# Performance work log

Measured on AMD Instinct MI355X. Metric: run time of the kernel, lower is better.

## Reference

```python
import jax, jax.numpy as jnp
import numpy as np

K = 100
TEMPERATURE = 1.0


def setup_inputs() -> dict:
    key = jax.random.key(0)
    k1, k2, k3 = jax.random.split(key, 3)
    student_emb = jax.random.normal(k1, (8, 512, 1500), dtype=jnp.float32)
    teacher_codes = jax.random.randint(k2, (8, 1500), 0, 4096, dtype=jnp.int64)
    codebook = jax.random.normal(k3, (4096, 512), dtype=jnp.float32)
    return {"student_emb": student_emb, "teacher_codes": teacher_codes, "codebook": codebook}


def reference(student_emb, teacher_codes, codebook):
    B, C, T = student_emb.shape
    # flatten tokens: (N, C) with N = B*T
    emb = jnp.transpose(student_emb, (0, 2, 1)).reshape(-1, C)
    codes = teacher_codes.reshape(-1).astype(jnp.int32)

    # Euclidean cdist via the ||a||^2 + ||b||^2 - 2ab expansion (same math as torch.cdist)
    emb_sq = jnp.sum(emb * emb, axis=1, keepdims=True)            # (N,1)
    cb_sq = jnp.sum(codebook * codebook, axis=1)[None, :]         # (1,V)
    d2 = emb_sq + cb_sq - 2.0 * jnp.matmul(emb, codebook.T)       # (N,V)
    distances = jnp.sqrt(jnp.maximum(d2, 0.0))

    # top-k smallest distances
    _, top_k_indices = jax.lax.top_k(-distances, K)               # (N,K)

    # include_correct: replace last candidate with the true code if absent
    correct_in_topk = jnp.any(top_k_indices == codes[:, None], axis=1)
    top_k_indices = top_k_indices.at[:, -1].set(
        jnp.where(correct_in_topk, top_k_indices[:, -1], codes))

    candidate_distances = jnp.take_along_axis(distances, top_k_indices, axis=1)
    logits = -candidate_distances / TEMPERATURE                   # (N,K)

    match = top_k_indices == codes[:, None]
    local_labels = jnp.argmax(match.astype(jnp.int32), axis=1)    # (N,)

    logp = jax.nn.log_softmax(logits, axis=1)
    loss = -jnp.mean(jnp.take_along_axis(logp, local_labels[:, None], axis=1))

    local_predictions = jnp.argmax(logits, axis=-1)
    local_accuracy = jnp.mean((local_predictions == local_labels).astype(jnp.float32))
    global_predictions = jnp.argmin(distances, axis=-1)
    global_accuracy = jnp.mean((global_predictions == codes).astype(jnp.float32))
    correct_in_candidates = jnp.mean(jnp.any(top_k_indices == codes[:, None], axis=1).astype(jnp.float32))

    return loss, local_accuracy, global_accuracy, correct_in_candidates
```

## Files before the change

kernel.cpp:

```cpp
#include <hip/hip_runtime.h>
#include <hip/hip_bf16.h>
#include <cstdint>

#define B_ 8
#define C_ 512
#define T_ 1500
#define N_ (B_*T_)
#define NPAD_ 12032
#define V_ 4096
#define K_ 100

typedef unsigned long long u64;
typedef __attribute__((ext_vector_type(8))) short short8;
typedef __attribute__((ext_vector_type(8))) unsigned short u16x8;
typedef __attribute__((ext_vector_type(4))) float f32x4;

__device__ __forceinline__ unsigned short f2bf(float x){
    __hip_bfloat16 h = __float2bfloat16(x);
    return __builtin_bit_cast(unsigned short, h);
}
__device__ __forceinline__ unsigned short f2h(float x){
    return __builtin_bit_cast(unsigned short, (_Float16)x);
}
__device__ __forceinline__ float h2f(unsigned short h){
    return (float)__builtin_bit_cast(_Float16, h);
}

__device__ __forceinline__ void gll16(const unsigned short* g, unsigned short* l){
    __builtin_amdgcn_global_load_lds(
        (const __attribute__((address_space(1))) void*)g,
        (__attribute__((address_space(3))) void*)l, 16, 0, 0);
}

__global__ __launch_bounds__(256) void cbconv_kernel(const float* __restrict__ CB,
                                                     unsigned short* __restrict__ CBh,
                                                     float* __restrict__ csq){
    int wv = threadIdx.x >> 6, lane = threadIdx.x & 63;
    int r = blockIdx.x * 4 + wv;
    const float4* p4 = (const float4*)(CB + (size_t)r * C_);
    ushort4* o4 = (ushort4*)(CBh + (size_t)r * C_);
    float s = 0.f;
    #pragma unroll
    for (int j = 0; j < 2; ++j){
        float4 v = p4[lane + j*64];
        s += v.x*v.x + v.y*v.y + v.z*v.z + v.w*v.w;
        ushort4 h; h.x = f2bf(v.x); h.y = f2bf(v.y); h.z = f2bf(v.z); h.w = f2bf(v.w);
        o4[lane + j*64] = h;
    }
    #pragma unroll
    for (int o = 32; o; o >>= 1) s += __shfl_down(s, o, 64);
    if (lane == 0) csq[r] = s;
}

__global__ __launch_bounds__(256) void transpose_conv_kernel(const float* __restrict__ S,
                                                             unsigned short* __restrict__ embT,
                                                             float* __restrict__ esq){
    __shared__ float tile[32][33];
    __shared__ float psum[8][33];
    int b  = blockIdx.z;
    int c0 = blockIdx.y * 32;
    int t0 = blockIdx.x * 32;
    int tx = threadIdx.x, ty = threadIdx.y;
    #pragma unroll
    for (int r = 0; r < 4; ++r){
        int c = c0 + ty + r*8;
        int t = t0 + tx;
        tile[ty + r*8][tx] = (t < T_) ? S[((size_t)b*C_ + c)*T_ + t] : 0.f;
    }
    __syncthreads();
    float ps = 0.f;
    #pragma unroll
    for (int r = 0; r < 4; ++r){ float v = tile[ty + r*8][tx]; ps += v * v; }
    psum[ty][tx] = ps;
    #pragma unroll
    for (int r = 0; r < 4; ++r){
        int t = t0 + ty + r*8;
        int c = c0 + tx;
        if (t < T_) embT[((size_t)b*T_ + t)*C_ + c] = f2bf(tile[tx][ty + r*8]);
    }
    __syncthreads();
    if (ty == 0){
        int t = t0 + tx;
        if (t < T_){
            float s2 = 0.f;
            #pragma unroll
            for (int w = 0; w < 8; ++w) s2 += psum[w][tx];
            atomicAdd(&esq[b*T_ + t], s2);
        }
    }
}

__global__ __launch_bounds__(256) void gemm_dot_kernel(
    const unsigned short* __restrict__ A, const unsigned short* __restrict__ Bm,
    unsigned short* __restrict__ doth, int row_lo, int row_hi)
{
    __shared__ unsigned short As[3][128*32];
    __shared__ unsigned short Bs[3][128*32];
    int tid = threadIdx.x, lane = tid & 63, wv = tid >> 6;
    int row0 = row_lo + blockIdx.x * 128;
    int col0 = blockIdx.y * 128;

    int sr = lane >> 2;
    int sk = (lane & 3) * 8;
    int ar0 = row0 + wv*32 + sr;       int ar1 = ar0 + 16;
    int ca0 = (ar0 < N_) ? ar0 : N_-1; int ca1 = (ar1 < N_) ? ar1 : N_-1;
    const unsigned short* Ap0 = A  + (size_t)ca0 * C_ + sk;
    const unsigned short* Ap1 = A  + (size_t)ca1 * C_ + sk;
    const unsigned short* Bp0 = Bm + (size_t)(col0 + wv*32 + sr) * C_ + sk;
    const unsigned short* Bp1 = Bp0 + (size_t)16 * C_;

    int wm = (wv >> 1) * 64, wn = (wv & 1) * 64;
    int fr = lane & 15;
    int fk = (lane >> 4) * 8;

    f32x4 acc[4][4];
    #pragma unroll
    for (int i = 0; i < 4; ++i)
        #pragma unroll
        for (int j = 0; j < 4; ++j) acc[i][j] = (f32x4){0.f, 0.f, 0.f, 0.f};

    auto stage = [&](int s, int kt){
        int k0 = kt * 32;
        gll16(Ap0 + k0, &As[s][(wv*32     ) * 32]);
        gll16(Ap1 + k0, &As[s][(wv*32 + 16) * 32]);
        gll16(Bp0 + k0, &Bs[s][(wv*32     ) * 32]);
        gll16(Bp1 + k0, &Bs[s][(wv*32 + 16) * 32]);
    };
    auto compute = [&](int s){
        short8 af[4], bf[4];
        #pragma unroll
        for (int i = 0; i < 4; ++i) af[i] = *(const short8*)&As[s][(wm + i*16 + fr)*32 + fk];
        #pragma unroll
        for (int j = 0; j < 4; ++j) bf[j] = *(const short8*)&Bs[s][(wn + j*16 + fr)*32 + fk];
        #pragma unroll
        for (int i = 0; i < 4; ++i)
            #pragma unroll
            for (int j = 0; j < 4; ++j)
                acc[i][j] = __builtin_amdgcn_mfma_f32_16x16x32_bf16(bf[j], af[i], acc[i][j], 0, 0, 0);
    };

    stage(0, 0);
    stage(1, 1);

    #pragma unroll
    for (int kt = 0; kt < 14; ++kt){
        asm volatile("s_waitcnt vmcnt(4)" ::: "memory");
        __builtin_amdgcn_s_barrier();
        asm volatile("" ::: "memory");
        stage((kt + 2) % 3, kt + 2);
        compute(kt % 3);
    }
    asm volatile("s_waitcnt vmcnt(4)" ::: "memory");
    __builtin_amdgcn_s_barrier();
    asm volatile("" ::: "memory");
    compute(14 % 3);
    asm volatile("s_waitcnt vmcnt(0)" ::: "memory");
    __builtin_amdgcn_s_barrier();
    asm volatile("" ::: "memory");
    compute(15 % 3);

    int en = lane & 15;
    int ev = (lane >> 4) * 4;
    #pragma unroll
    for (int i = 0; i < 4; ++i){
        int n = row0 + wm + i*16 + en;
        if (n >= row_hi) continue;
        size_t base = (size_t)(n - row_lo) * V_;
        int vb = col0 + wn + ev;
        #pragma unroll
        for (int j = 0; j < 4; ++j){
            ushort4 h;
            h.x = f2h(acc[i][j][0]);
            h.y = f2h(acc[i][j][1]);
            h.z = f2h(acc[i][j][2]);
            h.w = f2h(acc[i][j][3]);
            *(ushort4*)&doth[base + vb + j*16] = h;
        }
    }
}

__global__ __launch_bounds__(256, 2) void select_kernel(const unsigned short* __restrict__ doth,
                                                        const int* __restrict__ codes,
                                                        const float* __restrict__ esq,
                                                        const float* __restrict__ csq,
                                                        float2* __restrict__ pairbuf,
                                                        int row_lo, int nrows){
    int tid = threadIdx.x, lane = tid & 63, wv = tid >> 6;
    int lrow = blockIdx.x * 4 + wv;
    if (lrow >= nrows) return;
    int n = row_lo + lrow;
    const u16x8* r8 = (const u16x8*)(doth + (size_t)lrow * V_);

    __shared__ unsigned hist[4][256] __attribute__((aligned(16)));
    __shared__ unsigned coll[4][64];
    __shared__ unsigned collcnt[4];

    float esq_n = esq[n];
    int code = codes[n];
    float dotc = h2f(doth[(size_t)lrow * V_ + code]);
    unsigned ucode = __float_as_uint(fmaxf(esq_n + csq[code] - 2.f * dotc, 0.f));

    unsigned u[64];
    #pragma unroll
    for (int j = 0; j < 8; ++j){
        u16x8 h = r8[lane + j*64];
        const float4* cp = (const float4*)(csq + 8*lane + 512*j);
        float4 c0 = cp[0], c1 = cp[1];
        float cs[8] = {c0.x, c0.y, c0.z, c0.w, c1.x, c1.y, c1.z, c1.w};
        #pragma unroll
        for (int e = 0; e < 8; ++e){
            float d2 = fmaxf(esq_n + cs[e] - 2.f * h2f(h[e]), 0.f);
            u[8*j+e] = __float_as_uint(d2);
        }
    }

    unsigned umin = u[0], umax = u[0];
    #pragma unroll
    for (int k = 1; k < 64; ++k){
        umin = (u[k] < umin) ? u[k] : umin;
        umax = (u[k] > umax) ? u[k] : umax;
    }
    #pragma unroll
    for (int o = 32; o; o >>= 1){
        unsigned a = (unsigned)__shfl_xor((int)umin, o, 64); if (a < umin) umin = a;
        unsigned b = (unsigned)__shfl_xor((int)umax, o, 64); if (b > umax) umax = b;
    }
    unsigned im = 0xFFFFFFFFu;
    #pragma unroll
    for (int k = 0; k < 64; ++k){
        unsigned idx = 8u*(unsigned)lane + (unsigned)(512*(k >> 3) + (k & 7));
        if (u[k] == umin && idx < im) im = idx;
    }
    #pragma unroll
    for (int o = 32; o; o >>= 1){
        unsigned a = (unsigned)__shfl_xor((int)im, o, 64); if (a < im) im = a;
    }
    int idx0 = (int)im;
    float d0 = sqrtf(__uint_as_float(umin));

    unsigned t;
    if (umin == umax){
        t = umin;
    } else {
        ((uint4*)&hist[wv][0])[lane] = (uint4){0u,0u,0u,0u};
        if (lane == 0) collcnt[wv] = 0u;
        asm volatile("s_waitcnt lgkmcnt(0)" ::: "memory");
        float fmn = __uint_as_float(umin), fmx = __uint_as_float(umax);
        float invw = 256.0f / (fmx - fmn);
        #pragma unroll
        for (int k = 0; k < 64; ++k){
            float fk = __uint_as_float(u[k]);
            int b = (int)((fk - fmn) * invw); b = (b > 255) ? 255 : b;
            atomicAdd(&hist[wv][b], 1u);
        }
        asm volatile("s_waitcnt lgkmcnt(0)" ::: "memory");
        uint4 hq = ((uint4*)&hist[wv][0])[lane];
        unsigned lsum = hq.x + hq.y + hq.z + hq.w;
        unsigned inc = lsum;
        #pragma unroll
        for (int o = 1; o < 64; o <<= 1){
            unsigned y = (unsigned)__shfl_up((int)inc, o, 64);
            if (lane >= o) inc += y;
        }
        unsigned e0 = inc - lsum;
        unsigned e1 = e0 + hq.x, e2 = e1 + hq.y, e3 = e2 + hq.z, e4 = e3 + hq.w;
        int sel = -1;
        if      (e0 <= 99u && 99u < e1) sel = 0;
        else if (e1 <= 99u && 99u < e2) sel = 1;
        else if (e2 <= 99u && 99u < e3) sel = 2;
        else if (e3 <= 99u && 99u < e4) sel = 3;
        u64 bal = __ballot(sel >= 0);
        int src = __ffsll(bal) - 1;
        unsigned myBk = (unsigned)(4*lane + (sel < 0 ? 0 : sel));
        unsigned myBase = (sel == 1) ? e1 : (sel == 2) ? e2 : (sel == 3) ? e3 : e0;
        int Bk   = __shfl((int)myBk,   src, 64);
        int base = __shfl((int)myBase, src, 64);
        int rk = 99 - base;
        #pragma unroll
        for (int k = 0; k < 64; ++k){
            float fk = __uint_as_float(u[k]);
            int b = (int)((fk - fmn) * invw); b = (b > 255) ? 255 : b;
            if (b == Bk){
                unsigned pos = atomicAdd(&collcnt[wv], 1u);
                if (pos < 64u) coll[wv][pos] = u[k];
            }
        }
        asm volatile("s_waitcnt lgkmcnt(0)" ::: "memory");
        unsigned bcnt = collcnt[wv];
        if (bcnt <= 64u){
            unsigned w = (lane < (int)bcnt) ? coll[wv][lane] : 0xFFFFFFFFu;
            unsigned wmn = (lane < (int)bcnt) ? w : 0xFFFFFFFFu;
            unsigned wmx = (lane < (int)bcnt) ? w : 0u;
            #pragma unroll
            for (int o = 32; o; o >>= 1){
                unsigned a = (unsigned)__shfl_xor((int)wmn, o, 64); if (a < wmn) wmn = a;
                unsigned b = (unsigned)__shfl_xor((int)wmx, o, 64); if (b > wmx) wmx = b;
            }
            unsigned P;
            if (wmn == wmx) P = wmn;
            else {
                int hb = 31 - __clz((int)(wmn ^ wmx));
                unsigned mask = (hb == 31) ? 0xFFFFFFFFu : ((1u << (hb+1)) - 1u);
                P = wmn & ~mask;
                for (int b = hb; b >= 0; --b){
                    unsigned cand = P | (1u << b);
                    int c = __popcll(__ballot(w < cand));
                    if (c <= rk) P = cand;
                }
            }
            t = P;
        } else {
            int hb = 31 - __clz((int)(umin ^ umax));
            unsigned mask = (hb == 31) ? 0xFFFFFFFFu : ((1u << (hb+1)) - 1u);
            unsigned P = umin & ~mask;
            for (int b = hb; b >= 0; --b){
                unsigned cand = P | (1u << b);
                int c = 0;
                #pragma unroll
                for (int k = 0; k < 64; ++k) c += (u[k] < cand) ? 1 : 0;
                #pragma unroll
                for (int o = 32; o; o >>= 1) c += __shfl_xor(c, o, 64);
                if (c <= 99) P = cand;
            }
            t = P;
        }
    }
    float tval = sqrtf(__uint_as_float(t));

    float s = 0.f; int cl = 0;
    #pragma unroll
    for (int k = 0; k < 64; ++k){
        if (u[k] < t){ s += __expf(d0 - sqrtf(__uint_as_float(u[k]))); cl++; }
    }
    #pragma unroll
    for (int o = 32; o; o >>= 1){
        s += __shfl_xor(s, o, 64);
        cl += __shfl_xor(cl, o, 64);
    }
    if (lane == 0){
        float S = s + (float)(K_ - cl) * __expf(d0 - tval);
        float dcode = sqrtf(__uint_as_float(ucode));
        if (ucode > t) S += __expf(d0 - dcode) - __expf(d0 - tval);
        float nll = dcode - d0 + __logf(S);
        pairbuf[n] = make_float2(nll, (idx0 == code) ? 1.f : 0.f);
    }
}

__global__ __launch_bounds__(1024) void finalize_kernel(const float2* __restrict__ pair,
                                                        float* __restrict__ out){
    int tid = threadIdx.x;
    float sn = 0.f, sh = 0.f;
    for (int i = tid; i < N_; i += 1024){
        float2 p = pair[i]; sn += p.x; sh += p.y;
    }
    #pragma unroll
    for (int o = 32; o; o >>= 1){ sn += __shfl_down(sn, o, 64); sh += __shfl_down(sh, o, 64); }
    __shared__ float a[16], b[16];
    int wv = tid >> 6, lane = tid & 63;
    if (lane == 0){ a[wv] = sn; b[wv] = sh; }
    __syncthreads();
    if (tid == 0){
        float L = 0.f, H = 0.f;
        #pragma unroll
        for (int i = 0; i < 16; ++i){ L += a[i]; H += b[i]; }
        out[0] = L / (float)N_;
        out[1] = H / (float)N_;
        out[2] = H / (float)N_;
        out[3] = 1.0f;
    }
}

extern "C" void kernel_launch(void* const* d_in, const int* in_sizes, int n_in,
                              void* d_out, int out_size, void* d_ws, size_t ws_size,
                              hipStream_t stream){
    const float* S   = (const float*)d_in[0];
    const int* codes = (const int*)d_in[1];
    const float* CB  = (const float*)d_in[2];
    float* out = (float*)d_out;

    char* w = (char*)d_ws;
    size_t off = 0;
    unsigned short* embT = (unsigned short*)(w + off); off += (size_t)NPAD_ * C_ * 2;
    unsigned short* CBh  = (unsigned short*)(w + off); off += (size_t)V_ * C_ * 2;
    float* csq = (float*)(w + off); off += (size_t)V_ * 4;
    float* esq = (float*)(w + off); off += (size_t)N_ * 4;
    off = (off + 255) & ~(size_t)255;
    float2* pairbuf = (float2*)(w + off); off += (size_t)N_ * 8;
    unsigned short* dotbuf = (unsigned short*)(w + off);

    size_t avail = (ws_size > off) ? ws_size - off : 0;
    long maxrows = (long)(avail / ((size_t)V_ * 2));
    int chunk = (maxrows >= N_) ? N_ : (int)maxrows;
    if (chunk < 4) chunk = 4;

    hipMemsetAsync(esq, 0, (size_t)N_ * 4, stream);
    hipLaunchKernelGGL(cbconv_kernel, dim3(V_/4), dim3(256), 0, stream, CB, CBh, csq);
    hipLaunchKernelGGL(transpose_conv_kernel, dim3((T_+31)/32, C_/32, B_), dim3(32, 8), 0, stream,
                       S, embT, esq);

    for (int row_lo = 0; row_lo < N_; row_lo += chunk){
        int row_hi = row_lo + chunk; if (row_hi > N_) row_hi = N_;
        int rows = row_hi - row_lo;
        hipLaunchKernelGGL(gemm_dot_kernel, dim3((rows + 127)/128, V_/128), dim3(256), 0, stream,
                           embT, CBh, dotbuf, row_lo, row_hi);
        hipLaunchKernelGGL(select_kernel, dim3((rows + 3)/4), dim3(256), 0, stream,
                           dotbuf, codes, esq, csq, pairbuf, row_lo, rows);
    }
    hipLaunchKernelGGL(finalize_kernel, dim3(1), dim3(1024), 0, stream, pairbuf, out);
}
```

Measured before the change: 229.6 us.

## Enlarge GEMM tile to 256x256 with 8 waves, swizzled LDS and 4-stage pipeline

The bf16 distance GEMM moves from 128x128 tiles with 4 waves to 256x256 tiles with 8 waves, each wave computing a 128x64 sub-tile. It uses 128 KB of dynamic LDS with a 4-slot ring and an XOR swizzle on the k offset to avoid bank conflicts. Loads for A and B are interleaved between two half-MFMA phases, with barriers and s_setprio. The aim is better operand reuse and more MFMA issue relative to memory traffic. In exchange, the larger tile gives fewer blocks on a 12000-row problem, so partial tiles and wave quantization may hurt, along with higher register pressure and more barriers.

```diff
diff --git a/kernel.cpp b/kernel.cpp
--- a/kernel.cpp
+++ b/kernel.cpp
@@ -90,83 +90,99 @@
     }
 }
 
-__global__ __launch_bounds__(256) void gemm_dot_kernel(
+__global__ __launch_bounds__(512, 2) void gemm_dot_kernel(
     const unsigned short* __restrict__ A, const unsigned short* __restrict__ Bm,
     unsigned short* __restrict__ doth, int row_lo, int row_hi)
 {
-    __shared__ unsigned short As[3][128*32];
-    __shared__ unsigned short Bs[3][128*32];
+    extern __shared__ unsigned short lds[];
     int tid = threadIdx.x, lane = tid & 63, wv = tid >> 6;
-    int row0 = row_lo + blockIdx.x * 128;
-    int col0 = blockIdx.y * 128;
-
-    int sr = lane >> 2;
-    int sk = (lane & 3) * 8;
-    int ar0 = row0 + wv*32 + sr;       int ar1 = ar0 + 16;
-    int ca0 = (ar0 < N_) ? ar0 : N_-1; int ca1 = (ar1 < N_) ? ar1 : N_-1;
-    const unsigned short* Ap0 = A  + (size_t)ca0 * C_ + sk;
-    const unsigned short* Ap1 = A  + (size_t)ca1 * C_ + sk;
-    const unsigned short* Bp0 = Bm + (size_t)(col0 + wv*32 + sr) * C_ + sk;
-    const unsigned short* Bp1 = Bp0 + (size_t)16 * C_;
-
-    int wm = (wv >> 1) * 64, wn = (wv & 1) * 64;
+    int wm = wv >> 2, wn = wv & 3;
+    int row0 = row_lo + blockIdx.x * 256;
+    int col0 = blockIdx.y * 256;
+
+    int l2 = lane >> 2;
+    int swz = (((lane & 3) ^ (l2 & 3) ^ ((lane >> 4) & 3)) << 3);
+    const unsigned short* ApS[2]; const unsigned short* BpS[2];
+    #pragma unroll
+    for (int r = 0; r < 2; ++r){
+        int ra = row0 + r*128 + wv*16 + l2;
+        int ca = (ra < N_) ? ra : N_-1;
+        ApS[r] = A  + (size_t)ca * C_ + swz;
+        BpS[r] = Bm + (size_t)(col0 + r*128 + wv*16 + l2) * C_ + swz;
+    }
+
     int fr = lane & 15;
-    int fk = (lane >> 4) * 8;
-
-    f32x4 acc[4][4];
-    #pragma unroll
-    for (int i = 0; i < 4; ++i)
+    int q  = lane >> 4;
+    int rsw = ((q ^ (fr & 3) ^ ((fr >> 2) & 3)) << 3);
+    int aBase = (wm*128 + fr)*32 + rsw;
+    int bBase = 32768 + (wn*64 + fr)*32 + rsw;
+
+    f32x4 acc[8][4];
+    #pragma unroll
+    for (int i = 0; i < 8; ++i)
         #pragma unroll
         for (int j = 0; j < 4; ++j) acc[i][j] = (f32x4){0.f, 0.f, 0.f, 0.f};
 
-    auto stage = [&](int s, int kt){
-        int k0 = kt * 32;
-        gll16(Ap0 + k0, &As[s][(wv*32     ) * 32]);
-        gll16(Ap1 + k0, &As[s][(wv*32 + 16) * 32]);
-        gll16(Bp0 + k0, &Bs[s][(wv*32     ) * 32]);
-        gll16(Bp1 + k0, &Bs[s][(wv*32 + 16) * 32]);
+    auto stageA = [&](int kt){
+        int s = kt & 3, k0 = kt * 32;
+        gll16(ApS[0] + k0, &lds[s*8192 +        wv*512]);
+        gll16(ApS[1] + k0, &lds[s*8192 + 4096 + wv*512]);
     };
-    auto compute = [&](int s){
-        short8 af[4], bf[4];
-        #pragma unroll
-        for (int i = 0; i < 4; ++i) af[i] = *(const short8*)&As[s][(wm + i*16 + fr)*32 + fk];
-        #pragma unroll
-        for (int j = 0; j < 4; ++j) bf[j] = *(const short8*)&Bs[s][(wn + j*16 + fr)*32 + fk];
+    auto stageB = [&](int kt){
+        int s = kt & 3, k0 = kt * 32;
+        gll16(BpS[0] + k0, &lds[32768 + s*8192 +        wv*512]);
+        gll16(BpS[1] + k0, &lds[32768 + s*8192 + 4096 + wv*512]);
+    };
+
+    stageA(0); stageB(0);
+    stageA(1); stageB(1);
+    asm volatile("s_waitcnt vmcnt(4)" ::: "memory");
+    __builtin_amdgcn_s_barrier();
+
+    auto tile = [&](int kt, bool doStage, int vm){
+        int s = kt & 3;
+        const unsigned short* Al = &lds[s*8192 + aBase];
+        const unsigned short* Bl = &lds[s*8192 + bBase];
+        short8 a[4], b[4];
+        #pragma unroll
+        for (int j = 0; j < 4; ++j) b[j] = *(const short8*)(Bl + j*512);
+        #pragma unroll
+        for (int i = 0; i < 4; ++i) a[i] = *(const short8*)(Al + i*512);
+        if (doStage) stageA(kt + 2);
+        __builtin_amdgcn_s_barrier();
+        __builtin_amdgcn_s_setprio(1);
         #pragma unroll
         for (int i = 0; i < 4; ++i)
             #pragma unroll
             for (int j = 0; j < 4; ++j)
-                acc[i][j] = __builtin_amdgcn_mfma_f32_16x16x32_bf16(bf[j], af[i], acc[i][j], 0, 0, 0);
+                acc[i][j] = __builtin_amdgcn_mfma_f32_16x16x32_bf16(b[j], a[i], acc[i][j], 0, 0, 0);
+        __builtin_amdgcn_s_setprio(0);
+        __builtin_amdgcn_s_barrier();
+        #pragma unroll
+        for (int i = 0; i < 4; ++i) a[i] = *(const short8*)(Al + (4+i)*512);
+        if (doStage) stageB(kt + 2);
+        if (vm == 4) asm volatile("s_waitcnt vmcnt(4)" ::: "memory");
+        else if (vm == 0) asm volatile("s_waitcnt vmcnt(0)" ::: "memory");
+        __builtin_amdgcn_s_barrier();
+        __builtin_amdgcn_s_setprio(1);
+        #pragma unroll
+        for (int i = 0; i < 4; ++i)
+            #pragma unroll
+            for (int j = 0; j < 4; ++j)
+                acc[4+i][j] = __builtin_amdgcn_mfma_f32_16x16x32_bf16(b[j], a[i], acc[4+i][j], 0, 0, 0);
+        __builtin_amdgcn_s_setprio(0);
+        __builtin_amdgcn_s_barrier();
     };
 
-    stage(0, 0);
-    stage(1, 1);
-
-    #pragma unroll
-    for (int kt = 0; kt < 14; ++kt){
-        asm volatile("s_waitcnt vmcnt(4)" ::: "memory");
-        __builtin_amdgcn_s_barrier();
-        asm volatile("" ::: "memory");
-        stage((kt + 2) % 3, kt + 2);
-        compute(kt % 3);
-    }
-    asm volatile("s_waitcnt vmcnt(4)" ::: "memory");
-    __builtin_amdgcn_s_barrier();
-    asm volatile("" ::: "memory");
-    compute(14 % 3);
-    asm volatile("s_waitcnt vmcnt(0)" ::: "memory");
-    __builtin_amdgcn_s_barrier();
-    asm volatile("" ::: "memory");
-    compute(15 % 3);
-
-    int en = lane & 15;
-    int ev = (lane >> 4) * 4;
-    #pragma unroll
-    for (int i = 0; i < 4; ++i){
-        int n = row0 + wm + i*16 + en;
+    for (int kt = 0; kt < 14; ++kt) tile(kt, true, 4);
+    tile(14, false, 0);
+    tile(15, false, -1);
+
+    #pragma unroll
+    for (int i = 0; i < 8; ++i){
+        int n = row0 + wm*128 + i*16 + fr;
         if (n >= row_hi) continue;
-        size_t base = (size_t)(n - row_lo) * V_;
-        int vb = col0 + wn + ev;
+        size_t base = (size_t)(n - row_lo) * V_ + col0 + wn*64 + q*4;
         #pragma unroll
         for (int j = 0; j < 4; ++j){
             ushort4 h;
@@ -174,7 +190,7 @@
             h.y = f2h(acc[i][j][1]);
             h.z = f2h(acc[i][j][2]);
             h.w = f2h(acc[i][j][3]);
-            *(ushort4*)&doth[base + vb + j*16] = h;
+            *(ushort4*)&doth[base + j*16] = h;
         }
     }
 }
@@ -401,8 +417,8 @@
     for (int row_lo = 0; row_lo < N_; row_lo += chunk){
         int row_hi = row_lo + chunk; if (row_hi > N_) row_hi = N_;
         int rows = row_hi - row_lo;
-        hipLaunchKernelGGL(gemm_dot_kernel, dim3((rows + 127)/128, V_/128), dim3(256), 0, stream,
-                           embT, CBh, dotbuf, row_lo, row_hi);
+        hipLaunchKernelGGL(gemm_dot_kernel, dim3((rows + 255)/256, V_/256), dim3(512),
+                           131072, stream, embT, CBh, dotbuf, row_lo, row_hi);
         hipLaunchKernelGGL(select_kernel, dim3((rows + 3)/4), dim3(256), 0, stream,
                            dotbuf, codes, esq, csq, pairbuf, row_lo, rows);
     }
```

Result: no change. 227.7 us (-0.8%).
